# Optimization experiments

Hardware: AMD Instinct MI355X
Metric: run time of the kernel (lower is better)

## Reference

```python
import jax, jax.numpy as jnp
import numpy as np

N, K, D = 131072, 256, 128


def setup_inputs() -> dict:
    key = jax.random.key(0)
    k1, k2 = jax.random.split(key, 2)
    x = jax.random.normal(k1, (N, D), dtype=jnp.float32)
    mu = jax.random.normal(k2, (K, D), dtype=jnp.float32)
    prec = jnp.ones((D,), dtype=jnp.float32)
    return {"x": x, "mu": mu, "prec": prec}


def reference(x, mu, prec):
    # measure[n,k] = -0.5 * sum_d prec[d] * (x[n,d] - mu[k,d])**2
    # Expanded quadratic form avoids materializing the (N,K,D) diff tensor:
    #   sum_d prec*(x-mu)^2 = sum_d prec*x^2 - 2*sum_d (prec*x)*mu + sum_d prec*mu^2
    x_sq = jnp.einsum('nd,d->n', x * x, prec)            # (N,)
    mu_sq = jnp.einsum('kd,d->k', mu * mu, prec)         # (K,)
    cross = jnp.einsum('nd,d,kd->nk', x, prec, mu)       # (N,K)
    m = -0.5 * (x_sq[:, None] - 2.0 * cross + mu_sq[None, :])  # (N,K)
    return -jnp.sum(jax.nn.logsumexp(m, axis=1))
```

## Files before the change

### kernel.cpp

```cpp
#include <hip/hip_runtime.h>
#include <hip/hip_bf16.h>

#define N_ROWS 131072
#define K_MIX  256
#define D_DIM  128
#define LDSB_STRIDE 136
#define B_CHUNKS (K_MIX * LDSB_STRIDE / 8)

typedef float  f32x4  __attribute__((ext_vector_type(4)));
typedef short  bf16x8 __attribute__((ext_vector_type(8)));

__device__ inline bf16x8 pack8(float4 a, float4 b) {
    union { bf16x8 v; __hip_bfloat162 h[4]; } u;
    u.h[0] = __float22bfloat162_rn(make_float2(a.x, a.y));
    u.h[1] = __float22bfloat162_rn(make_float2(a.z, a.w));
    u.h[2] = __float22bfloat162_rn(make_float2(b.x, b.y));
    u.h[3] = __float22bfloat162_rn(make_float2(b.z, b.w));
    return u.v;
}

__global__ void prep_kernel(const float* __restrict__ mu,
                            const float* __restrict__ prec,
                            unsigned short* __restrict__ Bp,
                            float* __restrict__ musq)
{
    int idx = blockIdx.x * 256 + threadIdx.x;
    int row = idx >> 5;
    int c4  = idx & 31;
    float4 mv = ((const float4*)mu)[idx];
    float4 pv = ((const float4*)prec)[c4];
    float px = mv.x * pv.x, py = mv.y * pv.y, pz = mv.z * pv.z, pw = mv.w * pv.w;
    union { ushort4 u4; __hip_bfloat162 h[2]; } h;
    h.h[0] = __float22bfloat162_rn(make_float2(px, py));
    h.h[1] = __float22bfloat162_rn(make_float2(pz, pw));
    *(ushort4*)&Bp[row * LDSB_STRIDE + c4 * 4] = h.u4;
    if (c4 == 31) {
        bf16x8 z = (bf16x8)0;
        *(bf16x8*)&Bp[row * LDSB_STRIDE + 128] = z;
    }
    float ps = px * mv.x + py * mv.y + pz * mv.z + pw * mv.w;
    ps += __shfl_xor(ps, 1);  ps += __shfl_xor(ps, 2);
    ps += __shfl_xor(ps, 4);  ps += __shfl_xor(ps, 8);
    ps += __shfl_xor(ps, 16);
    if ((threadIdx.x & 31) == 0) musq[row] = 0.5f * ps;
}

__global__ __launch_bounds__(256, 2)
void mixture_main(const float* __restrict__ x,
                  const unsigned short* __restrict__ Bp,
                  const float* __restrict__ musqg,
                  const float* __restrict__ prec,
                  float* __restrict__ out)
{
    __shared__ __align__(16) unsigned short sB[K_MIX * LDSB_STRIDE];
    __shared__ float sMusq[K_MIX];
    __shared__ float sPrec[D_DIM];
    __shared__ float sRed[4];

    const int tid  = threadIdx.x;
    const int lane = tid & 63;
    const int wave = tid >> 6;
    const int low4 = lane & 15;
    const int q    = lane >> 4;

    {
        const bf16x8* src = (const bf16x8*)Bp;
        bf16x8* dst = (bf16x8*)sB;
        #pragma unroll
        for (int i = 0; i < B_CHUNKS / 256; ++i)
            dst[i * 256 + tid] = src[i * 256 + tid];
        sMusq[tid] = -musqg[tid];
        if (tid < D_DIM) sPrec[tid] = prec[tid];
    }
    __syncthreads();

    const float4* x4 = (const float4*)x;
    const int rbase = blockIdx.x * 256 + wave * 32;
    const float4* xr0 = x4 + (size_t)(rbase + low4) * 32;
    const float4* xr1 = x4 + (size_t)(rbase + low4 + 16) * 32;

    float lacc = 0.f;

    #pragma unroll 1
    for (int rg = 0; rg < 2; ++rg) {
        const float4* p0 = xr0 + rg * 128 * 32;
        const float4* p1 = xr1 + rg * 128 * 32;

        float4 xv[4][4];
        #pragma unroll
        for (int k = 0; k < 4; ++k) {
            const int d4 = k * 8 + q * 2;
            xv[k][0] = p0[d4]; xv[k][1] = p0[d4 + 1];
            xv[k][2] = p1[d4]; xv[k][3] = p1[d4 + 1];
        }

        float xsA = 0.f, xsB = 0.f;
        bf16x8 a0[4], a1[4];
        #pragma unroll
        for (int k = 0; k < 4; ++k) {
            const int d4 = k * 8 + q * 2;
            float4 pa = *(const float4*)&sPrec[d4 * 4];
            float4 pb = *(const float4*)&sPrec[d4 * 4 + 4];
            xsA += pa.x*xv[k][0].x*xv[k][0].x + pa.y*xv[k][0].y*xv[k][0].y
                 + pa.z*xv[k][0].z*xv[k][0].z + pa.w*xv[k][0].w*xv[k][0].w;
            xsB += pb.x*xv[k][1].x*xv[k][1].x + pb.y*xv[k][1].y*xv[k][1].y
                 + pb.z*xv[k][1].z*xv[k][1].z + pb.w*xv[k][1].w*xv[k][1].w;
            xsA += pa.x*xv[k][2].x*xv[k][2].x + pa.y*xv[k][2].y*xv[k][2].y
                 + pa.z*xv[k][2].z*xv[k][2].z + pa.w*xv[k][2].w*xv[k][2].w;
            xsB += pb.x*xv[k][3].x*xv[k][3].x + pb.y*xv[k][3].y*xv[k][3].y
                 + pb.z*xv[k][3].z*xv[k][3].z + pb.w*xv[k][3].w*xv[k][3].w;
            a0[k] = pack8(xv[k][0], xv[k][1]);
            a1[k] = pack8(xv[k][2], xv[k][3]);
        }

        float m_run[2][4], s_run[2][4];
        #pragma unroll
        for (int m = 0; m < 2; ++m)
            #pragma unroll
            for (int i = 0; i < 4; ++i) { m_run[m][i] = -3.0e38f; s_run[m][i] = 0.f; }

        #pragma unroll 1
        for (int h = 0; h < 2; ++h) {
            f32x4 acc[2][8];
            #pragma unroll
            for (int c = 0; c < 8; ++c) {
                float mneg = sMusq[(h * 8 + c) * 16 + low4];
                #pragma unroll
                for (int i = 0; i < 4; ++i) { acc[0][c][i] = mneg; acc[1][c][i] = mneg; }
            }

            #pragma unroll
            for (int k = 0; k < 4; ++k) {
                #pragma unroll
                for (int c = 0; c < 8; ++c) {
                    const unsigned short* bp =
                        &sB[((h * 8 + c) * 16 + low4) * LDSB_STRIDE + k * 32 + q * 8];
                    bf16x8 b = *(const bf16x8*)bp;
                    acc[0][c] = __builtin_amdgcn_mfma_f32_16x16x32_bf16(a0[k], b, acc[0][c], 0, 0, 0);
                    acc[1][c] = __builtin_amdgcn_mfma_f32_16x16x32_bf16(a1[k], b, acc[1][c], 0, 0, 0);
                }
            }

            #pragma unroll
            for (int m = 0; m < 2; ++m) {
                #pragma unroll
                for (int i = 0; i < 4; ++i) {
                    float v0 = acc[m][0][i], v1 = acc[m][1][i];
                    float v2 = acc[m][2][i], v3 = acc[m][3][i];
                    float v4 = acc[m][4][i], v5 = acc[m][5][i];
                    float v6 = acc[m][6][i], v7 = acc[m][7][i];
                    float hmax = fmaxf(fmaxf(fmaxf(v0, v1), fmaxf(v2, v3)),
                                       fmaxf(fmaxf(v4, v5), fmaxf(v6, v7)));
                    float hsum = __expf(v0 - hmax) + __expf(v1 - hmax)
                               + __expf(v2 - hmax) + __expf(v3 - hmax)
                               + __expf(v4 - hmax) + __expf(v5 - hmax)
                               + __expf(v6 - hmax) + __expf(v7 - hmax);
                    float mr = m_run[m][i];
                    float mn = fmaxf(mr, hmax);
                    s_run[m][i] = s_run[m][i] * __expf(mr - mn) + hsum * __expf(hmax - mn);
                    m_run[m][i] = mn;
                }
            }
        }

        #pragma unroll
        for (int m = 0; m < 2; ++m) {
            #pragma unroll
            for (int i = 0; i < 4; ++i) {
                float mr = m_run[m][i], sr = s_run[m][i];
                #pragma unroll
                for (int step = 1; step <= 8; step <<= 1) {
                    float mo = __shfl_xor(mr, step);
                    float so = __shfl_xor(sr, step);
                    float mn = fmaxf(mr, mo);
                    sr = sr * __expf(mr - mn) + so * __expf(mo - mn);
                    mr = mn;
                }
                if (low4 == 0) lacc -= mr + __logf(sr);
            }
        }
        lacc += 0.5f * (xsA + xsB);
    }

    lacc += __shfl_xor(lacc, 32); lacc += __shfl_xor(lacc, 16);
    lacc += __shfl_xor(lacc, 8);  lacc += __shfl_xor(lacc, 4);
    lacc += __shfl_xor(lacc, 2);  lacc += __shfl_xor(lacc, 1);
    if (lane == 0) sRed[wave] = lacc;
    __syncthreads();
    if (tid == 0) atomicAdd(out, sRed[0] + sRed[1] + sRed[2] + sRed[3]);
}

extern "C" void kernel_launch(void* const* d_in, const int* in_sizes, int n_in,
                              void* d_out, int out_size, void* d_ws, size_t ws_size,
                              hipStream_t stream) {
    const float* x    = (const float*)d_in[0];
    const float* mu   = (const float*)d_in[1];
    const float* prec = (const float*)d_in[2];
    float* out = (float*)d_out;

    unsigned short* Bp = (unsigned short*)d_ws;
    float* musq = (float*)((char*)d_ws + K_MIX * LDSB_STRIDE * 2);

    hipMemsetAsync(d_out, 0, sizeof(float), stream);
    prep_kernel<<<32, 256, 0, stream>>>(mu, prec, Bp, musq);
    mixture_main<<<N_ROWS / 256, 256, 0, stream>>>(x, Bp, musq, prec, out);
}
```

Measured before the change: 112.0 us.

## Prefetch x ahead of compute, async LDS load of B, use exp2 domain

Issues the global loads for the first row group before the B-matrix staging, and copies B into LDS with direct global-to-LDS loads instead of going through registers. The second row group's x rows are prefetched into registers while the first group's MFMA and softmax work runs. The log2(e) factor is folded into the precomputed mu and musq so the loop can call exp2 directly, the first half initializes the running max without a rescale, and ln2 is applied only at the end. This is meant to hide global-memory latency and trim transcendental work, at the cost of more live registers, which could reduce occupancy.

```diff
diff --git a/kernel.cpp b/kernel.cpp
--- a/kernel.cpp
+++ b/kernel.cpp
@@ -6,6 +6,8 @@
 #define D_DIM  128
 #define LDSB_STRIDE 136
 #define B_CHUNKS (K_MIX * LDSB_STRIDE / 8)
+#define LOG2E 1.4426950408889634f
+#define LN2   0.6931471805599453f
 
 typedef float  f32x4  __attribute__((ext_vector_type(4)));
 typedef short  bf16x8 __attribute__((ext_vector_type(8)));
@@ -31,8 +33,8 @@
     float4 pv = ((const float4*)prec)[c4];
     float px = mv.x * pv.x, py = mv.y * pv.y, pz = mv.z * pv.z, pw = mv.w * pv.w;
     union { ushort4 u4; __hip_bfloat162 h[2]; } h;
-    h.h[0] = __float22bfloat162_rn(make_float2(px, py));
-    h.h[1] = __float22bfloat162_rn(make_float2(pz, pw));
+    h.h[0] = __float22bfloat162_rn(make_float2(px * LOG2E, py * LOG2E));
+    h.h[1] = __float22bfloat162_rn(make_float2(pz * LOG2E, pw * LOG2E));
     *(ushort4*)&Bp[row * LDSB_STRIDE + c4 * 4] = h.u4;
     if (c4 == 31) {
         bf16x8 z = (bf16x8)0;
@@ -42,7 +44,83 @@
     ps += __shfl_xor(ps, 1);  ps += __shfl_xor(ps, 2);
     ps += __shfl_xor(ps, 4);  ps += __shfl_xor(ps, 8);
     ps += __shfl_xor(ps, 16);
-    if ((threadIdx.x & 31) == 0) musq[row] = 0.5f * ps;
+    if ((threadIdx.x & 31) == 0) musq[row] = 0.5f * LOG2E * ps;
+}
+
+__device__ inline float do_rowgroup(const bf16x8* a0, const bf16x8* a1,
+                                    const unsigned short* sB, const float* sMusq,
+                                    int low4, int q)
+{
+    float m_run[2][4], s_run[2][4];
+
+    #pragma unroll 1
+    for (int h = 0; h < 2; ++h) {
+        f32x4 acc[2][8];
+        #pragma unroll
+        for (int c = 0; c < 8; ++c) {
+            float mneg = sMusq[(h * 8 + c) * 16 + low4];
+            #pragma unroll
+            for (int i = 0; i < 4; ++i) { acc[0][c][i] = mneg; acc[1][c][i] = mneg; }
+        }
+
+        #pragma unroll
+        for (int k = 0; k < 4; ++k) {
+            #pragma unroll
+            for (int c = 0; c < 8; ++c) {
+                const unsigned short* bp =
+                    &sB[((h * 8 + c) * 16 + low4) * LDSB_STRIDE + k * 32 + q * 8];
+                bf16x8 b = *(const bf16x8*)bp;
+                acc[0][c] = __builtin_amdgcn_mfma_f32_16x16x32_bf16(a0[k], b, acc[0][c], 0, 0, 0);
+                acc[1][c] = __builtin_amdgcn_mfma_f32_16x16x32_bf16(a1[k], b, acc[1][c], 0, 0, 0);
+            }
+        }
+
+        #pragma unroll
+        for (int m = 0; m < 2; ++m) {
+            #pragma unroll
+            for (int i = 0; i < 4; ++i) {
+                float v0 = acc[m][0][i], v1 = acc[m][1][i];
+                float v2 = acc[m][2][i], v3 = acc[m][3][i];
+                float v4 = acc[m][4][i], v5 = acc[m][5][i];
+                float v6 = acc[m][6][i], v7 = acc[m][7][i];
+                float hmax = fmaxf(fmaxf(fmaxf(v0, v1), fmaxf(v2, v3)),
+                                   fmaxf(fmaxf(v4, v5), fmaxf(v6, v7)));
+                float hsum = __builtin_amdgcn_exp2f(v0 - hmax) + __builtin_amdgcn_exp2f(v1 - hmax)
+                           + __builtin_amdgcn_exp2f(v2 - hmax) + __builtin_amdgcn_exp2f(v3 - hmax)
+                           + __builtin_amdgcn_exp2f(v4 - hmax) + __builtin_amdgcn_exp2f(v5 - hmax)
+                           + __builtin_amdgcn_exp2f(v6 - hmax) + __builtin_amdgcn_exp2f(v7 - hmax);
+                if (h == 0) {
+                    m_run[m][i] = hmax; s_run[m][i] = hsum;
+                } else {
+                    float mr = m_run[m][i];
+                    float mn = fmaxf(mr, hmax);
+                    s_run[m][i] = s_run[m][i] * __builtin_amdgcn_exp2f(mr - mn)
+                                + hsum        * __builtin_amdgcn_exp2f(hmax - mn);
+                    m_run[m][i] = mn;
+                }
+            }
+        }
+    }
+
+    float lsum = 0.f;
+    #pragma unroll
+    for (int m = 0; m < 2; ++m) {
+        #pragma unroll
+        for (int i = 0; i < 4; ++i) {
+            float mr = m_run[m][i], sr = s_run[m][i];
+            #pragma unroll
+            for (int step = 1; step <= 8; step <<= 1) {
+                float mo = __shfl_xor(mr, step);
+                float so = __shfl_xor(sr, step);
+                float mn = fmaxf(mr, mo);
+                sr = sr * __builtin_amdgcn_exp2f(mr - mn)
+                   + so * __builtin_amdgcn_exp2f(mo - mn);
+                mr = mn;
+            }
+            if (low4 == 0) lsum += LN2 * (mr + __builtin_amdgcn_logf(sr));
+        }
+    }
+    return lsum;
 }
 
 __global__ __launch_bounds__(256, 2)
@@ -63,124 +141,89 @@
     const int low4 = lane & 15;
     const int q    = lane >> 4;
 
+    const float4* x4 = (const float4*)x;
+    const int rbase = blockIdx.x * 256 + wave * 32;
+    const float4* p0g0 = x4 + (size_t)(rbase + low4) * 32;
+    const float4* p1g0 = p0g0 + 16 * 32;
+    const float4* p0g1 = p0g0 + 128 * 32;
+    const float4* p1g1 = p1g0 + 128 * 32;
+
+    float4 xv[4][4];
+    #pragma unroll
+    for (int k = 0; k < 4; ++k) {
+        const int d4 = k * 8 + q * 2;
+        xv[k][0] = p0g0[d4]; xv[k][1] = p0g0[d4 + 1];
+        xv[k][2] = p1g0[d4]; xv[k][3] = p1g0[d4 + 1];
+    }
+
     {
-        const bf16x8* src = (const bf16x8*)Bp;
-        bf16x8* dst = (bf16x8*)sB;
-        #pragma unroll
-        for (int i = 0; i < B_CHUNKS / 256; ++i)
-            dst[i * 256 + tid] = src[i * 256 + tid];
+        #pragma unroll
+        for (int i = 0; i < B_CHUNKS / 256; ++i) {
+            const int chunk = i * 256 + wave * 64;
+            const unsigned short* g = Bp + (size_t)(chunk + lane) * 8;
+            unsigned short* l = sB + (size_t)(chunk + lane) * 8;
+            __builtin_amdgcn_global_load_lds(
+                (const __attribute__((address_space(1))) unsigned int*)g,
+                (__attribute__((address_space(3))) unsigned int*)l,
+                16, 0, 0);
+        }
         sMusq[tid] = -musqg[tid];
         if (tid < D_DIM) sPrec[tid] = prec[tid];
     }
     __syncthreads();
 
-    const float4* x4 = (const float4*)x;
-    const int rbase = blockIdx.x * 256 + wave * 32;
-    const float4* xr0 = x4 + (size_t)(rbase + low4) * 32;
-    const float4* xr1 = x4 + (size_t)(rbase + low4 + 16) * 32;
-
     float lacc = 0.f;
 
-    #pragma unroll 1
-    for (int rg = 0; rg < 2; ++rg) {
-        const float4* p0 = xr0 + rg * 128 * 32;
-        const float4* p1 = xr1 + rg * 128 * 32;
-
-        float4 xv[4][4];
-        #pragma unroll
-        for (int k = 0; k < 4; ++k) {
-            const int d4 = k * 8 + q * 2;
-            xv[k][0] = p0[d4]; xv[k][1] = p0[d4 + 1];
-            xv[k][2] = p1[d4]; xv[k][3] = p1[d4 + 1];
-        }
-
-        float xsA = 0.f, xsB = 0.f;
-        bf16x8 a0[4], a1[4];
-        #pragma unroll
-        for (int k = 0; k < 4; ++k) {
-            const int d4 = k * 8 + q * 2;
-            float4 pa = *(const float4*)&sPrec[d4 * 4];
-            float4 pb = *(const float4*)&sPrec[d4 * 4 + 4];
-            xsA += pa.x*xv[k][0].x*xv[k][0].x + pa.y*xv[k][0].y*xv[k][0].y
-                 + pa.z*xv[k][0].z*xv[k][0].z + pa.w*xv[k][0].w*xv[k][0].w;
-            xsB += pb.x*xv[k][1].x*xv[k][1].x + pb.y*xv[k][1].y*xv[k][1].y
-                 + pb.z*xv[k][1].z*xv[k][1].z + pb.w*xv[k][1].w*xv[k][1].w;
-            xsA += pa.x*xv[k][2].x*xv[k][2].x + pa.y*xv[k][2].y*xv[k][2].y
-                 + pa.z*xv[k][2].z*xv[k][2].z + pa.w*xv[k][2].w*xv[k][2].w;
-            xsB += pb.x*xv[k][3].x*xv[k][3].x + pb.y*xv[k][3].y*xv[k][3].y
-                 + pb.z*xv[k][3].z*xv[k][3].z + pb.w*xv[k][3].w*xv[k][3].w;
-            a0[k] = pack8(xv[k][0], xv[k][1]);
-            a1[k] = pack8(xv[k][2], xv[k][3]);
-        }
-
-        float m_run[2][4], s_run[2][4];
-        #pragma unroll
-        for (int m = 0; m < 2; ++m)
-            #pragma unroll
-            for (int i = 0; i < 4; ++i) { m_run[m][i] = -3.0e38f; s_run[m][i] = 0.f; }
-
-        #pragma unroll 1
-        for (int h = 0; h < 2; ++h) {
-            f32x4 acc[2][8];
-            #pragma unroll
-            for (int c = 0; c < 8; ++c) {
-                float mneg = sMusq[(h * 8 + c) * 16 + low4];
-                #pragma unroll
-                for (int i = 0; i < 4; ++i) { acc[0][c][i] = mneg; acc[1][c][i] = mneg; }
-            }
-
-            #pragma unroll
-            for (int k = 0; k < 4; ++k) {
-                #pragma unroll
-                for (int c = 0; c < 8; ++c) {
-                    const unsigned short* bp =
-                        &sB[((h * 8 + c) * 16 + low4) * LDSB_STRIDE + k * 32 + q * 8];
-                    bf16x8 b = *(const bf16x8*)bp;
-                    acc[0][c] = __builtin_amdgcn_mfma_f32_16x16x32_bf16(a0[k], b, acc[0][c], 0, 0, 0);
-                    acc[1][c] = __builtin_amdgcn_mfma_f32_16x16x32_bf16(a1[k], b, acc[1][c], 0, 0, 0);
-                }
-            }
-
-            #pragma unroll
-            for (int m = 0; m < 2; ++m) {
-                #pragma unroll
-                for (int i = 0; i < 4; ++i) {
-                    float v0 = acc[m][0][i], v1 = acc[m][1][i];
-                    float v2 = acc[m][2][i], v3 = acc[m][3][i];
-                    float v4 = acc[m][4][i], v5 = acc[m][5][i];
-                    float v6 = acc[m][6][i], v7 = acc[m][7][i];
-                    float hmax = fmaxf(fmaxf(fmaxf(v0, v1), fmaxf(v2, v3)),
-                                       fmaxf(fmaxf(v4, v5), fmaxf(v6, v7)));
-                    float hsum = __expf(v0 - hmax) + __expf(v1 - hmax)
-                               + __expf(v2 - hmax) + __expf(v3 - hmax)
-                               + __expf(v4 - hmax) + __expf(v5 - hmax)
-                               + __expf(v6 - hmax) + __expf(v7 - hmax);
-                    float mr = m_run[m][i];
-                    float mn = fmaxf(mr, hmax);
-                    s_run[m][i] = s_run[m][i] * __expf(mr - mn) + hsum * __expf(hmax - mn);
-                    m_run[m][i] = mn;
-                }
-            }
-        }
-
-        #pragma unroll
-        for (int m = 0; m < 2; ++m) {
-            #pragma unroll
-            for (int i = 0; i < 4; ++i) {
-                float mr = m_run[m][i], sr = s_run[m][i];
-                #pragma unroll
-                for (int step = 1; step <= 8; step <<= 1) {
-                    float mo = __shfl_xor(mr, step);
-                    float so = __shfl_xor(sr, step);
-                    float mn = fmaxf(mr, mo);
-                    sr = sr * __expf(mr - mn) + so * __expf(mo - mn);
-                    mr = mn;
-                }
-                if (low4 == 0) lacc -= mr + __logf(sr);
-            }
-        }
-        lacc += 0.5f * (xsA + xsB);
-    }
+    float xsA = 0.f, xsB = 0.f;
+    bf16x8 a0[4], a1[4];
+    #pragma unroll
+    for (int k = 0; k < 4; ++k) {
+        const int d4 = k * 8 + q * 2;
+        float4 pa = *(const float4*)&sPrec[d4 * 4];
+        float4 pb = *(const float4*)&sPrec[d4 * 4 + 4];
+        xsA += pa.x*xv[k][0].x*xv[k][0].x + pa.y*xv[k][0].y*xv[k][0].y
+             + pa.z*xv[k][0].z*xv[k][0].z + pa.w*xv[k][0].w*xv[k][0].w;
+        xsB += pb.x*xv[k][1].x*xv[k][1].x + pb.y*xv[k][1].y*xv[k][1].y
+             + pb.z*xv[k][1].z*xv[k][1].z + pb.w*xv[k][1].w*xv[k][1].w;
+        xsA += pa.x*xv[k][2].x*xv[k][2].x + pa.y*xv[k][2].y*xv[k][2].y
+             + pa.z*xv[k][2].z*xv[k][2].z + pa.w*xv[k][2].w*xv[k][2].w;
+        xsB += pb.x*xv[k][3].x*xv[k][3].x + pb.y*xv[k][3].y*xv[k][3].y
+             + pb.z*xv[k][3].z*xv[k][3].z + pb.w*xv[k][3].w*xv[k][3].w;
+        a0[k] = pack8(xv[k][0], xv[k][1]);
+        a1[k] = pack8(xv[k][2], xv[k][3]);
+    }
+    lacc += 0.5f * (xsA + xsB);
+
+    float4 xw[4][4];
+    #pragma unroll
+    for (int k = 0; k < 4; ++k) {
+        const int d4 = k * 8 + q * 2;
+        xw[k][0] = p0g1[d4]; xw[k][1] = p0g1[d4 + 1];
+        xw[k][2] = p1g1[d4]; xw[k][3] = p1g1[d4 + 1];
+    }
+
+    lacc -= do_rowgroup(a0, a1, sB, sMusq, low4, q);
+
+    xsA = 0.f; xsB = 0.f;
+    #pragma unroll
+    for (int k = 0; k < 4; ++k) {
+        const int d4 = k * 8 + q * 2;
+        float4 pa = *(const float4*)&sPrec[d4 * 4];
+        float4 pb = *(const float4*)&sPrec[d4 * 4 + 4];
+        xsA += pa.x*xw[k][0].x*xw[k][0].x + pa.y*xw[k][0].y*xw[k][0].y
+             + pa.z*xw[k][0].z*xw[k][0].z + pa.w*xw[k][0].w*xw[k][0].w;
+        xsB += pb.x*xw[k][1].x*xw[k][1].x + pb.y*xw[k][1].y*xw[k][1].y
+             + pb.z*xw[k][1].z*xw[k][1].z + pb.w*xw[k][1].w*xw[k][1].w;
+        xsA += pa.x*xw[k][2].x*xw[k][2].x + pa.y*xw[k][2].y*xw[k][2].y
+             + pa.z*xw[k][2].z*xw[k][2].z + pa.w*xw[k][2].w*xw[k][2].w;
+        xsB += pb.x*xw[k][3].x*xw[k][3].x + pb.y*xw[k][3].y*xw[k][3].y
+             + pb.z*xw[k][3].z*xw[k][3].z + pb.w*xw[k][3].w*xw[k][3].w;
+        a0[k] = pack8(xw[k][0], xw[k][1]);
+        a1[k] = pack8(xw[k][2], xw[k][3]);
+    }
+    lacc += 0.5f * (xsA + xsB);
+
+    lacc -= do_rowgroup(a0, a1, sB, sMusq, low4, q);
 
     lacc += __shfl_xor(lacc, 32); lacc += __shfl_xor(lacc, 16);
     lacc += __shfl_xor(lacc, 8);  lacc += __shfl_xor(lacc, 4);
```

Result: slower. 142.5 us (+27.2%).
